# Performance work log

Measured on AMD Instinct MI355X. Metric: run time of the kernel, lower is better.

The kernel has to match this reference:

```python
import jax, jax.numpy as jnp
import numpy as np

BINS = 10
LOSS_WEIGHT = 1.0


def setup_inputs() -> dict:
    key = jax.random.key(0)
    k1, k2, k3 = jax.random.split(key, 3)
    N, C = 262144, 80
    pred = jax.random.normal(k1, (N, C), dtype=jnp.float32)
    # binary class targets (sparse positives, as in detection)
    target = (jax.random.uniform(k2, (N, C)) < 0.02).astype(jnp.float32)
    # 1 = valid sample, 0 = ignored
    label_weight = (jax.random.uniform(k3, (N, C)) < 0.95).astype(jnp.float32)
    return {"pred": pred, "target": target, "label_weight": label_weight}


def reference(pred, target, label_weight):
    # GHM-C loss, momentum=0 path (no EMA buffer).
    valid = label_weight > 0
    validf = valid.astype(jnp.float32)
    tot = jnp.maximum(jnp.sum(validf), 1.0)

    # gradient norm g = |sigmoid(pred).detach() - target|, in [0, 1]
    g = jnp.abs(jax.lax.stop_gradient(jax.nn.sigmoid(pred)) - target)
    # edges are i/BINS with last edge 1+1e-6, so bin i covers [i/B, (i+1)/B);
    # equivalent to floor(g*B) clipped to [0, B-1] (g==1 lands in last bin).
    bin_idx = jnp.clip(jnp.floor(g * BINS).astype(jnp.int32), 0, BINS - 1)

    # per-bin counts over valid elements (single-pass histogram)
    counts = jax.ops.segment_sum(validf.reshape(-1), bin_idx.reshape(-1),
                                 num_segments=BINS)
    n = jnp.sum(counts > 0).astype(jnp.float32)  # number of non-empty bins
    per_bin_w = jnp.where(counts > 0, tot / jnp.maximum(counts, 1.0), 0.0)
    weights = per_bin_w[bin_idx] * validf  # scattered weight assignment
    weights = jnp.where(n > 0, weights / n, weights)

    # binary_cross_entropy_with_logits, elementwise: softplus(x) - x*t
    bce = jax.nn.softplus(pred) - pred * target
    loss = jnp.sum(bce * weights) / tot
    return loss * LOSS_WEIGHT
```

## Files before the change

kernel.cpp:

```cpp
#include <hip/hip_runtime.h>

#define BINS 10
#define TPB  256


__global__ __launch_bounds__(64) void ghmc_zero(float* ws_sum, int* ws_cnt) {
    int i = threadIdx.x;
    if (i < BINS) { ws_sum[i] = 0.0f; ws_cnt[i] = 0; }
}

#define GHMC_ELEM(pk, tk, wk)                                                 \
    do {                                                                      \
        float tm_ = __builtin_fmaf((tk), -2.0f, 1.0f);      \
        float y_  = tm_ * (pk);                                               \
        bool  v_  = ((wk) > 0.0f);                                            \
        float ye_ = v_ ? y_ : -60.0f;                                         \
        float e_  = __expf(-__builtin_fabsf(ye_));                 \
        float onep_ = 1.0f + e_;                        \
        float bce_  = __builtin_fmaf(0.69314718055994530942f,                 \
                                     __log2f(onep_),                          \
                                     __builtin_fmaxf(ye_, 0.0f));             \
        S[0] += bce_;                                                         \
        C0   += v_ ? 1 : 0;                                                   \
        _Pragma("unroll")                                                     \
        for (int b_ = 1; b_ <= 5; ++b_) {                                     \
            bool ge_ = (ye_ >= kL[b_ - 1]);                                   \
            S[b_] += ge_ ? bce_ : 0.0f;                                       \
            cLo   += ge_ ? (1u << (6 * (b_ - 1))) : 0u;                       \
        }                                                                     \
        _Pragma("unroll")                                                     \
        for (int b_ = 6; b_ <= 9; ++b_) {                                     \
            bool ge_ = (ye_ >= kL[b_ - 1]);                                   \
            S[b_] += ge_ ? bce_ : 0.0f;                                       \
            cHi   += ge_ ? (1u << (6 * (b_ - 6))) : 0u;                       \
        }                                                                     \
    } while (0)

__global__ __launch_bounds__(256) void ghmc_main(
    const float* __restrict__ pred, const float* __restrict__ targ,
    const float* __restrict__ lw,
    float* __restrict__ ws_sum, int* __restrict__ ws_cnt, int n) {

    const float kL[9] = { -2.1972246f, -1.3862944f, -0.84729786f, -0.40546511f,
                          0.0f, 0.40546511f, 0.84729786f, 1.3862944f, 2.1972246f };

    float S[BINS];
#pragma unroll
    for (int b = 0; b < BINS; ++b) S[b] = 0.0f;
    int C0 = 0;
    unsigned cLo = 0u, cHi = 0u;

    const int nvec = n >> 2;
    const int start = (int)(((long long)nvec * blockIdx.x) / gridDim.x);
    const int end   = (int)(((long long)nvec * (blockIdx.x + 1)) / gridDim.x);

    const float4* p4 = (const float4*)pred;
    const float4* t4 = (const float4*)targ;
    const float4* w4 = (const float4*)lw;

    int i = start + (int)threadIdx.x;
    if (i < end) {
        float4 p = p4[i], t = t4[i], w = w4[i];
        for (int j = i + TPB; j < end; j += TPB) {
            float4 pn = p4[j], tn = t4[j], wn = w4[j];
            GHMC_ELEM(p.x, t.x, w.x);
            GHMC_ELEM(p.y, t.y, w.y);
            GHMC_ELEM(p.z, t.z, w.z);
            GHMC_ELEM(p.w, t.w, w.w);
            p = pn; t = tn; w = wn;
        }
        GHMC_ELEM(p.x, t.x, w.x);
        GHMC_ELEM(p.y, t.y, w.y);
        GHMC_ELEM(p.z, t.z, w.z);
        GHMC_ELEM(p.w, t.w, w.w);
    }
    {
        int rem  = n & 3;
        int gtid = blockIdx.x * TPB + (int)threadIdx.x;
        if (gtid < rem) {
            int idx = (nvec << 2) + gtid;
            float pk = pred[idx], tk = targ[idx], wk = lw[idx];
            GHMC_ELEM(pk, tk, wk);
        }
    }

    float lsum[BINS];
    int   lcnt[BINS];
    {
        int Cc[BINS];
        Cc[0] = C0;
#pragma unroll
        for (int b = 1; b <= 5; ++b) Cc[b] = (int)((cLo >> (6 * (b - 1))) & 63u);
#pragma unroll
        for (int b = 6; b <= 9; ++b) Cc[b] = (int)((cHi >> (6 * (b - 6))) & 63u);
#pragma unroll
        for (int b = 0; b < BINS - 1; ++b) {
            lsum[b] = S[b] - S[b + 1];
            lcnt[b] = Cc[b] - Cc[b + 1];
        }
        lsum[BINS - 1] = S[BINS - 1];
        lcnt[BINS - 1] = Cc[BINS - 1];
    }

    __shared__ float s_bsum[BINS];
    __shared__ int   s_bcnt[BINS];
    if (threadIdx.x < BINS) { s_bsum[threadIdx.x] = 0.0f; s_bcnt[threadIdx.x] = 0; }
    __syncthreads();

    const int lane = threadIdx.x & 63;
#pragma unroll
    for (int b = 0; b < BINS; ++b) {
        float s = lsum[b];
        int   c = lcnt[b];
#pragma unroll
        for (int off = 32; off > 0; off >>= 1) {
            s += __shfl_xor(s, off, 64);
            c += __shfl_xor(c, off, 64);
        }
        if (lane == 0 && c != 0) {
            atomicAdd(&s_bsum[b], s);
            atomicAdd(&s_bcnt[b], c);
        }
    }
    __syncthreads();

    if (threadIdx.x < BINS) {
        float s = s_bsum[threadIdx.x];
        int   c = s_bcnt[threadIdx.x];
        if (c != 0) {
            atomicAdd(&ws_sum[threadIdx.x], s);
            atomicAdd(&ws_cnt[threadIdx.x], c);
        }
    }
}

__global__ __launch_bounds__(64) void ghmc_finalize(
    const float* __restrict__ ws_sum, const int* __restrict__ ws_cnt,
    float* __restrict__ out) {
    if (threadIdx.x == 0) {
        float acc = 0.0f;
        int nb = 0;
        for (int b = 0; b < BINS; ++b) {
            int c = ws_cnt[b];
            if (c > 0) { nb += 1; acc += ws_sum[b] / (float)c; }
        }
        out[0] = (nb > 0) ? (acc / (float)nb) : 0.0f;
    }
}

extern "C" void kernel_launch(void* const* d_in, const int* in_sizes, int n_in,
                              void* d_out, int out_size, void* d_ws, size_t ws_size,
                              hipStream_t stream) {
    const float* pred = (const float*)d_in[0];
    const float* targ = (const float*)d_in[1];
    const float* lw   = (const float*)d_in[2];
    float* out = (float*)d_out;
    const int n = in_sizes[0];

    float* ws_sum = (float*)d_ws;
    int*   ws_cnt = (int*)((char*)d_ws + BINS * sizeof(float));

    ghmc_zero<<<1, 64, 0, stream>>>(ws_sum, ws_cnt);

    const int threads = TPB;
    const int blocks  = 2048;
    ghmc_main<<<blocks, threads, 0, stream>>>(pred, targ, lw, ws_sum, ws_cnt, n);

    ghmc_finalize<<<1, 64, 0, stream>>>(ws_sum, ws_cnt, out);
}
```

Before: 257.3 us.

## Fuse finalize via last-block ticket, deepen prefetch, double grid size

Removes the separate finalize kernel: the last block to take an atomic ticket reads the global bin sums and writes the loss. The main loop now keeps two float4 tiles in flight instead of one, to hide more memory latency, and the grid grows from 2048 to 4096 blocks with a launch-bounds occupancy hint. This saves one kernel launch and should raise achieved bandwidth, at the cost of more registers per thread and twice as many global atomics.

```diff
diff --git a/kernel.cpp b/kernel.cpp
--- a/kernel.cpp
+++ b/kernel.cpp
@@ -2,11 +2,12 @@
 
 #define BINS 10
 #define TPB  256
+#define NBLK 4096
 
 
-__global__ __launch_bounds__(64) void ghmc_zero(float* ws_sum, int* ws_cnt) {
+__global__ __launch_bounds__(64) void ghmc_zero(unsigned* ws) {
     int i = threadIdx.x;
-    if (i < BINS) { ws_sum[i] = 0.0f; ws_cnt[i] = 0; }
+    if (i < 1 + 2 * BINS) ws[i] = 0u;
 }
 
 #define GHMC_ELEM(pk, tk, wk)                                                 \
@@ -36,10 +37,19 @@
         }                                                                     \
     } while (0)
 
-__global__ __launch_bounds__(256) void ghmc_main(
+#define GHMC_ELEM4(P, T, W)                                                   \
+    do {                                                                      \
+        GHMC_ELEM((P).x, (T).x, (W).x);                                       \
+        GHMC_ELEM((P).y, (T).y, (W).y);                                       \
+        GHMC_ELEM((P).z, (T).z, (W).z);                                       \
+        GHMC_ELEM((P).w, (T).w, (W).w);                                       \
+    } while (0)
+
+__global__ __launch_bounds__(256, 8) void ghmc_main(
     const float* __restrict__ pred, const float* __restrict__ targ,
     const float* __restrict__ lw,
-    float* __restrict__ ws_sum, int* __restrict__ ws_cnt, int n) {
+    unsigned* __restrict__ ticket, float* __restrict__ bsum,
+    int* __restrict__ bcnt, float* __restrict__ out, int n) {
 
     const float kL[9] = { -2.1972246f, -1.3862944f, -0.84729786f, -0.40546511f,
                           0.0f, 0.40546511f, 0.84729786f, 1.3862944f, 2.1972246f };
@@ -58,22 +68,23 @@
     const float4* t4 = (const float4*)targ;
     const float4* w4 = (const float4*)lw;
 
-    int i = start + (int)threadIdx.x;
-    if (i < end) {
-        float4 p = p4[i], t = t4[i], w = w4[i];
-        for (int j = i + TPB; j < end; j += TPB) {
-            float4 pn = p4[j], tn = t4[j], wn = w4[j];
-            GHMC_ELEM(p.x, t.x, w.x);
-            GHMC_ELEM(p.y, t.y, w.y);
-            GHMC_ELEM(p.z, t.z, w.z);
-            GHMC_ELEM(p.w, t.w, w.w);
-            p = pn; t = tn; w = wn;
-        }
-        GHMC_ELEM(p.x, t.x, w.x);
-        GHMC_ELEM(p.y, t.y, w.y);
-        GHMC_ELEM(p.z, t.z, w.z);
-        GHMC_ELEM(p.w, t.w, w.w);
+    const int i0 = start + (int)threadIdx.x;
+    float4 p0, t0, w0, p1, t1, w1;
+    const bool h0 = (i0 < end);
+    if (h0) { p0 = p4[i0]; t0 = t4[i0]; w0 = w4[i0]; }
+    const int i1 = i0 + TPB;
+    const bool h1 = (i1 < end);
+    if (h1) { p1 = p4[i1]; t1 = t4[i1]; w1 = w4[i1]; }
+
+    for (int j = i0 + 2 * TPB; j < end; j += TPB) {
+        float4 pn = p4[j], tn = t4[j], wn = w4[j];
+        GHMC_ELEM4(p0, t0, w0);
+        p0 = p1; t0 = t1; w0 = w1;
+        p1 = pn; t1 = tn; w1 = wn;
     }
+    if (h0) GHMC_ELEM4(p0, t0, w0);
+    if (h1) GHMC_ELEM4(p1, t1, w1);
+
     {
         int rem  = n & 3;
         int gtid = blockIdx.x * TPB + (int)threadIdx.x;
@@ -104,6 +115,7 @@
 
     __shared__ float s_bsum[BINS];
     __shared__ int   s_bcnt[BINS];
+    __shared__ int   s_last;
     if (threadIdx.x < BINS) { s_bsum[threadIdx.x] = 0.0f; s_bcnt[threadIdx.x] = 0; }
     __syncthreads();
 
@@ -128,21 +140,31 @@
         float s = s_bsum[threadIdx.x];
         int   c = s_bcnt[threadIdx.x];
         if (c != 0) {
-            atomicAdd(&ws_sum[threadIdx.x], s);
-            atomicAdd(&ws_cnt[threadIdx.x], c);
+            atomicAdd(&bsum[threadIdx.x], s);
+            atomicAdd(&bcnt[threadIdx.x], c);
         }
     }
-}
+    __threadfence();
+    __syncthreads();
 
-__global__ __launch_bounds__(64) void ghmc_finalize(
-    const float* __restrict__ ws_sum, const int* __restrict__ ws_cnt,
-    float* __restrict__ out) {
     if (threadIdx.x == 0) {
+        unsigned old = atomicAdd(ticket, 1u);
+        s_last = (old == (unsigned)(gridDim.x - 1)) ? 1 : 0;
+    }
+    __syncthreads();
+
+    if (s_last && threadIdx.x == 0) {
+        __threadfence();
         float acc = 0.0f;
         int nb = 0;
+#pragma unroll
         for (int b = 0; b < BINS; ++b) {
-            int c = ws_cnt[b];
-            if (c > 0) { nb += 1; acc += ws_sum[b] / (float)c; }
+            int c = atomicAdd(&bcnt[b], 0);
+            if (c > 0) {
+                float s = atomicAdd(&bsum[b], 0.0f);
+                nb += 1;
+                acc += s / (float)c;
+            }
         }
         out[0] = (nb > 0) ? (acc / (float)nb) : 0.0f;
     }
@@ -157,14 +179,12 @@
     float* out = (float*)d_out;
     const int n = in_sizes[0];
 
-    float* ws_sum = (float*)d_ws;
-    int*   ws_cnt = (int*)((char*)d_ws + BINS * sizeof(float));
+    unsigned* ticket = (unsigned*)d_ws;
+    float*    bsum   = (float*)((char*)d_ws + 4);
+    int*      bcnt   = (int*)((char*)d_ws + 4 + BINS * sizeof(float));
 
-    ghmc_zero<<<1, 64, 0, stream>>>(ws_sum, ws_cnt);
+    ghmc_zero<<<1, 64, 0, stream>>>((unsigned*)d_ws);
 
-    const int threads = TPB;
-    const int blocks  = 2048;
-    ghmc_main<<<blocks, threads, 0, stream>>>(pred, targ, lw, ws_sum, ws_cnt, n);
-
-    ghmc_finalize<<<1, 64, 0, stream>>>(ws_sum, ws_cnt, out);
+    ghmc_main<<<NBLK, TPB, 0, stream>>>(pred, targ, lw,
+                                        ticket, bsum, bcnt, out, n);
 }
```

Result: slower. 908.0 us (+252.9%).
